# Kernel optimization log

Hardware: AMD Instinct MI355X
Metric: run time of the kernel (lower is better)

Reference implementation:

```python
import jax, jax.numpy as jnp
import numpy as np


def setup_inputs() -> dict:
    key = jax.random.key(0)
    k1, k2 = jax.random.split(key)
    n, c, h, w = 8, 2048, 64, 64
    out_c = 512
    fea = jax.random.normal(k1, (n, c, h, w), dtype=jnp.float32)
    # Conv2d weight [out, in, kh=1, kw=9]; kaiming-ish scale
    W = jax.random.normal(k2, (out_c, c, 1, 9), dtype=jnp.float32) * 0.02
    b = jnp.zeros((out_c,), dtype=jnp.float32)
    return {"fea": fea, "W": W, "b": b}


def reference(fea, W, b):
    # Original module (stride=1 path): for each width column i, take the
    # [n,c,h,1] slice, run Conv2d(kernel=(1,9), pad=(0,4)) + ReLU, concat on w.
    # For a width-1 input, only the CENTER kernel tap (kw index 4) overlaps
    # real data; all other taps see zero padding. Hence each column output is
    # ReLU(W[:,:,0,4] @ column + b), and the concat over columns is exactly a
    # pointwise (1x1) conv over the full feature map with the center tap.
    Wc = W[:, :, 0, 4]  # [out_c, in_c]
    out = jnp.einsum('nchw,oc->nohw', fea, Wc) + b[None, :, None, None]
    return jax.nn.relu(out)
```

## Files before the change

### kernel.cpp

```cpp
#include <hip/hip_runtime.h>
#include <hip/hip_bf16.h>

typedef __bf16 bf16x8 __attribute__((ext_vector_type(8)));
typedef float floatx4 __attribute__((ext_vector_type(4)));

#define KDIM 2048
#define MDIM 512
#define HWDIM 4096
#define BN 128
#define BK 64
#define NITER (KDIM / BK)

__global__ void extract_w_kernel(const float* __restrict__ W, __bf16* __restrict__ Wc) {
  const int idx = blockIdx.x * 256 + threadIdx.x;
  const float4 v = ((const float4*)W)[idx];
  const float vv[4] = {v.x, v.y, v.z, v.w};
  const int f0 = idx * 4;
#pragma unroll
  for (int j = 0; j < 4; ++j) {
    const int f = f0 + j;
    if (f % 9 == 4) Wc[f / 9] = (__bf16)vv[j];
  }
}

__global__ __launch_bounds__(1024, 4) void conv1x1_kernel(
    const float* __restrict__ fea, const __bf16* __restrict__ Wc,
    const float* __restrict__ bias, float* __restrict__ out) {
  __shared__ __align__(16) __bf16 Bs[2][BN * BK];

  const int t    = threadIdx.x;
  const int wave = t >> 6;
  const int lane = t & 63;
  const int l15  = lane & 15;
  const int quad = lane >> 4;
  const int wm   = wave * 32;

  const int img = blockIdx.x >> 5;
  const int nb  = blockIdx.x & 31;

  const float* feaN = fea + (size_t)img * KDIM * HWDIM + (size_t)nb * BN;
  float*       outN = out + (size_t)img * MDIM * HWDIM + (size_t)nb * BN;

  const int hw   = lane + ((wave & 1) << 6);
  const int g    = wave >> 1;
  const int boff = hw * BK + ((g ^ (hw & 7)) * 8);
  const float* bsrc = feaN + (size_t)g * 8 * HWDIM + hw;

  const __bf16* aptr = Wc + (size_t)(wm + l15) * KDIM + quad * 8;

  float bpf[2][8];
  floatx4 acc[2][8];
#pragma unroll
  for (int i = 0; i < 2; ++i)
#pragma unroll
    for (int j = 0; j < 8; ++j) acc[i][j] = (floatx4){0.f, 0.f, 0.f, 0.f};

#pragma unroll
  for (int j = 0; j < 8; ++j)
    bpf[0][j] = __builtin_nontemporal_load(bsrc + (size_t)j * HWDIM);
#pragma unroll
  for (int j = 0; j < 8; ++j)
    bpf[1][j] = __builtin_nontemporal_load(bsrc + (size_t)(BK + j) * HWDIM);
  {
    bf16x8 h0;
#pragma unroll
    for (int j = 0; j < 8; ++j) h0[j] = (__bf16)bpf[0][j];
    *(bf16x8*)&Bs[0][boff] = h0;
  }
  __syncthreads();

#define KBODY(I, CUR)                                                          \
  {                                                                            \
    const int i_ = (I);                                                        \
    bf16x8 af[2][2];                                                           \
    const __bf16* ap = aptr + (size_t)i_ * BK;                                 \
    _Pragma("unroll")                                                          \
    for (int s = 0; s < 2; ++s)                                                \
      _Pragma("unroll")                                                        \
      for (int mt = 0; mt < 2; ++mt)                                           \
        af[s][mt] = *(const bf16x8*)(ap + (size_t)(mt * 16) * KDIM + s * 32);  \
    if (i_ + 1 < NITER) {                                                      \
      bf16x8 hn;                                                               \
      _Pragma("unroll")                                                        \
      for (int j = 0; j < 8; ++j) hn[j] = (__bf16)bpf[(CUR) ^ 1][j];           \
      *(bf16x8*)&Bs[(CUR) ^ 1][boff] = hn;                                     \
    }                                                                          \
    if (i_ + 2 < NITER) {                                                      \
      const float* p = bsrc + (size_t)(i_ + 2) * BK * HWDIM;                   \
      _Pragma("unroll")                                                        \
      for (int j = 0; j < 8; ++j)                                              \
        bpf[(CUR)][j] = __builtin_nontemporal_load(p + (size_t)j * HWDIM);     \
    }                                                                          \
    _Pragma("unroll")                                                          \
    for (int s = 0; s < 2; ++s)                                                \
      _Pragma("unroll")                                                        \
      for (int nt = 0; nt < 8; ++nt) {                                         \
        const int n_ = nt * 16 + l15;                                          \
        const bf16x8 bfr = *(const bf16x8*)&Bs[(CUR)][n_ * BK +                \
                              (((s * 4 + quad) ^ (n_ & 7)) * 8)];              \
        _Pragma("unroll")                                                      \
        for (int mt = 0; mt < 2; ++mt)                                         \
          acc[mt][nt] = __builtin_amdgcn_mfma_f32_16x16x32_bf16(af[s][mt],     \
                            bfr, acc[mt][nt], 0, 0, 0);                        \
      }                                                                        \
    __syncthreads();                                                           \
  }

  for (int i = 0; i < NITER; i += 2) {
    KBODY(i, 0)
    KBODY(i + 1, 1)
  }
#undef KBODY

#pragma unroll
  for (int mt = 0; mt < 2; ++mt) {
    const int o0 = wm + mt * 16 + quad * 4;
    const float4 bv = *(const float4*)(bias + o0);
    const float bvr[4] = {bv.x, bv.y, bv.z, bv.w};
#pragma unroll
    for (int r = 0; r < 4; ++r) {
      const size_t ro = (size_t)(o0 + r) * HWDIM;
#pragma unroll
      for (int nt = 0; nt < 8; ++nt) {
        float x = acc[mt][nt][r] + bvr[r];
        x = x > 0.f ? x : 0.f;
        __builtin_nontemporal_store(x, &outN[ro + nt * 16 + l15]);
      }
    }
  }
}

extern "C" void kernel_launch(void* const* d_in, const int* in_sizes, int n_in,
                              void* d_out, int out_size, void* d_ws, size_t ws_size,
                              hipStream_t stream) {
  const float* fea  = (const float*)d_in[0];
  const float* W    = (const float*)d_in[1];
  const float* bias = (const float*)d_in[2];
  float* out = (float*)d_out;
  __bf16* Wc = (__bf16*)d_ws;

  hipLaunchKernelGGL(extract_w_kernel, dim3(9216), dim3(256), 0, stream, W, Wc);
  hipLaunchKernelGGL(conv1x1_kernel, dim3(256), dim3(1024), 0, stream, fea, Wc, bias, out);
}
```

Baseline: 456.6 us.

## Split output channels across two blocks with XCD-aware tile mapping and smaller K step

The kernel now launches 512 blocks of 512 threads instead of 256 blocks of 1024 threads. Each block computes half of the output channels (BM=256) for one spatial tile, and the K step drops from 64 to 32 with a matching LDS swizzle. Block indices are remapped so the two channel-halves that read the same feature tile run on the same XCD. Nontemporal loads are replaced with normal loads so the second half can hit in L2. The aim is more blocks in flight per CU and better latency hiding, at the cost of reading each feature tile twice and more syncs per unit of work.

```diff
diff --git a/kernel.cpp b/kernel.cpp
--- a/kernel.cpp
+++ b/kernel.cpp
@@ -8,7 +8,8 @@
 #define MDIM 512
 #define HWDIM 4096
 #define BN 128
-#define BK 64
+#define BM 256
+#define BK 32
 #define NITER (KDIM / BK)
 
 __global__ void extract_w_kernel(const float* __restrict__ W, __bf16* __restrict__ Wc) {
@@ -23,7 +24,7 @@
   }
 }
 
-__global__ __launch_bounds__(1024, 4) void conv1x1_kernel(
+__global__ __launch_bounds__(512, 4) void conv1x1_kernel(
     const float* __restrict__ fea, const __bf16* __restrict__ Wc,
     const float* __restrict__ bias, float* __restrict__ out) {
   __shared__ __align__(16) __bf16 Bs[2][BN * BK];
@@ -33,17 +34,22 @@
   const int lane = t & 63;
   const int l15  = lane & 15;
   const int quad = lane >> 4;
-  const int wm   = wave * 32;
 
-  const int img = blockIdx.x >> 5;
-  const int nb  = blockIdx.x & 31;
+  const int xcd   = blockIdx.x & 7;
+  const int slot  = blockIdx.x >> 3;
+  const int tile  = xcd * 32 + (slot >> 1);
+  const int mhalf = slot & 1;
+  const int img   = tile >> 5;
+  const int nb    = tile & 31;
+
+  const int wm = mhalf * BM + wave * 32;
 
   const float* feaN = fea + (size_t)img * KDIM * HWDIM + (size_t)nb * BN;
   float*       outN = out + (size_t)img * MDIM * HWDIM + (size_t)nb * BN;
 
   const int hw   = lane + ((wave & 1) << 6);
   const int g    = wave >> 1;
-  const int boff = hw * BK + ((g ^ (hw & 7)) * 8);
+  const int boff = hw * BK + (((g + (hw >> 1)) & 3) * 8);
   const float* bsrc = feaN + (size_t)g * 8 * HWDIM + hw;
 
   const __bf16* aptr = Wc + (size_t)(wm + l15) * KDIM + quad * 8;
@@ -56,11 +62,9 @@
     for (int j = 0; j < 8; ++j) acc[i][j] = (floatx4){0.f, 0.f, 0.f, 0.f};
 
 #pragma unroll
-  for (int j = 0; j < 8; ++j)
-    bpf[0][j] = __builtin_nontemporal_load(bsrc + (size_t)j * HWDIM);
+  for (int j = 0; j < 8; ++j) bpf[0][j] = bsrc[(size_t)j * HWDIM];
 #pragma unroll
-  for (int j = 0; j < 8; ++j)
-    bpf[1][j] = __builtin_nontemporal_load(bsrc + (size_t)(BK + j) * HWDIM);
+  for (int j = 0; j < 8; ++j) bpf[1][j] = bsrc[(size_t)(BK + j) * HWDIM];
   {
     bf16x8 h0;
 #pragma unroll
@@ -72,13 +76,11 @@
 #define KBODY(I, CUR)                                                          \
   {                                                                            \
     const int i_ = (I);                                                        \
-    bf16x8 af[2][2];                                                           \
+    bf16x8 af[2];                                                              \
     const __bf16* ap = aptr + (size_t)i_ * BK;                                 \
     _Pragma("unroll")                                                          \
-    for (int s = 0; s < 2; ++s)                                                \
-      _Pragma("unroll")                                                        \
-      for (int mt = 0; mt < 2; ++mt)                                           \
-        af[s][mt] = *(const bf16x8*)(ap + (size_t)(mt * 16) * KDIM + s * 32);  \
+    for (int mt = 0; mt < 2; ++mt)                                             \
+      af[mt] = *(const bf16x8*)(ap + (size_t)(mt * 16) * KDIM);                \
     if (i_ + 1 < NITER) {                                                      \
       bf16x8 hn;                                                               \
       _Pragma("unroll")                                                        \
@@ -88,21 +90,18 @@
     if (i_ + 2 < NITER) {                                                      \
       const float* p = bsrc + (size_t)(i_ + 2) * BK * HWDIM;                   \
       _Pragma("unroll")                                                        \
-      for (int j = 0; j < 8; ++j)                                              \
-        bpf[(CUR)][j] = __builtin_nontemporal_load(p + (size_t)j * HWDIM);     \
+      for (int j = 0; j < 8; ++j) bpf[(CUR)][j] = p[(size_t)j * HWDIM];        \
     }                                                                          \
     _Pragma("unroll")                                                          \
-    for (int s = 0; s < 2; ++s)                                                \
+    for (int nt = 0; nt < 8; ++nt) {                                           \
+      const int n_ = nt * 16 + l15;                                            \
+      const bf16x8 bfr = *(const bf16x8*)&Bs[(CUR)][n_ * BK +                  \
+                            (((quad + (n_ >> 1)) & 3) * 8)];                   \
       _Pragma("unroll")                                                        \
-      for (int nt = 0; nt < 8; ++nt) {                                         \
-        const int n_ = nt * 16 + l15;                                          \
-        const bf16x8 bfr = *(const bf16x8*)&Bs[(CUR)][n_ * BK +                \
-                              (((s * 4 + quad) ^ (n_ & 7)) * 8)];              \
-        _Pragma("unroll")                                                      \
-        for (int mt = 0; mt < 2; ++mt)                                         \
-          acc[mt][nt] = __builtin_amdgcn_mfma_f32_16x16x32_bf16(af[s][mt],     \
-                            bfr, acc[mt][nt], 0, 0, 0);                        \
-      }                                                                        \
+      for (int mt = 0; mt < 2; ++mt)                                           \
+        acc[mt][nt] = __builtin_amdgcn_mfma_f32_16x16x32_bf16(af[mt], bfr,     \
+                          acc[mt][nt], 0, 0, 0);                               \
+    }                                                                          \
     __syncthreads();                                                           \
   }
 
@@ -140,5 +139,5 @@
   __bf16* Wc = (__bf16*)d_ws;
 
   hipLaunchKernelGGL(extract_w_kernel, dim3(9216), dim3(256), 0, stream, W, Wc);
-  hipLaunchKernelGGL(conv1x1_kernel, dim3(256), dim3(1024), 0, stream, fea, Wc, bias, out);
+  hipLaunchKernelGGL(conv1x1_kernel, dim3(512), dim3(512), 0, stream, fea, Wc, bias, out);
 }
```

Measured after the change: 437.4 us. -4.2%, faster.
